# Kernel optimization log

Measured on AMD Instinct MI355X. Metric: run time of the kernel, lower is better.

Reference implementation:

```python
import jax, jax.numpy as jnp
import numpy as np

NUM_USERS = 100000
NUM_ITEMS = 50000
N_NODES = NUM_USERS + NUM_ITEMS
EMBED_K = 64
N_LAYERS = 3
N_EDGES = 2000000
BATCH = 4096
EPS = 1e-12
NEG_SLOPE = 0.01  # torch.nn.functional.leaky_relu default


def setup_inputs() -> dict:
    key = jax.random.key(0)
    ks = jax.random.split(key, 12)
    return {
        "Gu": jax.random.normal(ks[0], (NUM_USERS, EMBED_K), jnp.float32) * 0.1,
        "Gi": jax.random.normal(ks[1], (NUM_ITEMS, EMBED_K), jnp.float32) * 0.1,
        "W1": jax.random.normal(ks[2], (N_LAYERS, EMBED_K, EMBED_K), jnp.float32) * 0.1,
        "b1": jax.random.normal(ks[3], (N_LAYERS, EMBED_K), jnp.float32) * 0.1,
        "W2": jax.random.normal(ks[4], (N_LAYERS, EMBED_K, EMBED_K), jnp.float32) * 0.1,
        "b2": jax.random.normal(ks[5], (N_LAYERS, EMBED_K), jnp.float32) * 0.1,
        "edge_w": jax.random.uniform(ks[6], (N_EDGES,), jnp.float32),
        "edge_src": jax.random.randint(ks[7], (N_EDGES,), 0, N_NODES, jnp.int32),
        "edge_dst": jax.random.randint(ks[8], (N_EDGES,), 0, N_NODES, jnp.int32),
        "user": jax.random.randint(ks[9], (BATCH,), 0, NUM_USERS, jnp.int32),
        "pos": jax.random.randint(ks[10], (BATCH,), 0, NUM_ITEMS, jnp.int32),
    }


def _propagate(Gu, Gi, W1, b1, W2, b2, edge_w, edge_src, edge_dst):
    # ego embeddings: concat users then items -> [N, d]
    x = jnp.concatenate([Gu, Gi], axis=0)
    embs = [x]
    for l in range(N_LAYERS):
        xj = x[edge_src]                       # [E, d] source (neighbor) feats
        xi = x[edge_dst]                       # [E, d] destination feats
        # NGCF message: norm * (lin1(x_j) + lin2(x_j * x_i))
        msg = (xj @ W1[l] + b1[l]) + ((xj * xi) @ W2[l] + b2[l])
        msg = msg * edge_w[:, None]
        agg = jax.ops.segment_sum(msg, edge_dst, num_segments=N_NODES)
        # update: aggregated messages + self transform, then LeakyReLU
        out = jax.nn.leaky_relu(agg + x @ W1[l] + b1[l], negative_slope=NEG_SLOPE)
        # message dropout is identity in eval mode; then row-wise L2 normalize
        nrm = jnp.sqrt(jnp.sum(out * out, axis=1, keepdims=True))
        x = out / jnp.maximum(nrm, EPS)
        embs.append(x)
    all_e = jnp.concatenate(embs, axis=1)      # [N, d*(L+1)]
    return all_e[:NUM_USERS], all_e[NUM_USERS:]


def reference(Gu, Gi, W1, b1, W2, b2, edge_w, edge_src, edge_dst, user, pos):
    gu, gi = _propagate(Gu, Gi, W1, b1, W2, b2, edge_w, edge_src, edge_dst)
    gamma_u = gu[user]                         # [B, d*(L+1)]
    gamma_i = gi[pos]
    xui = jnp.sum(gamma_u * gamma_i, axis=1)   # [B]
    return xui
```

## Files before the change

### kernel.cpp

```cpp
#include <hip/hip_runtime.h>


#define SCAN_TILE 4096
#define LAYER_GRID 1536

__global__ __launch_bounds__(256) void init_x_kernel(
    const float* __restrict__ Gu, const float* __restrict__ Gi,
    float* __restrict__ x, int nu4, int nt4) {
  int i = blockIdx.x * 256 + threadIdx.x;
  if (i >= nt4) return;
  float4 v = (i < nu4) ? ((const float4*)Gu)[i] : ((const float4*)Gi)[i - nu4];
  ((float4*)x)[i] = v;
}

__global__ __launch_bounds__(256) void hist_kernel(
    const int* __restrict__ dst, int* __restrict__ counts, int E) {
  int e = blockIdx.x * 256 + threadIdx.x;
  if (e >= E) return;
  atomicAdd(&counts[dst[e]], 1);
}

__global__ __launch_bounds__(256) void tile_sum_kernel(
    const int* __restrict__ counts, int* __restrict__ tsum, int n) {
  int tid = threadIdx.x;
  int lo = blockIdx.x * SCAN_TILE + tid * 16;
  int s = 0;
  if (lo + 16 <= n) {
    const int4* p = (const int4*)(counts + lo);
#pragma unroll
    for (int q = 0; q < 4; ++q) {
      int4 v = p[q];
      s += v.x + v.y + v.z + v.w;
    }
  } else {
    for (int i = lo; i < n && i < lo + 16; ++i) s += counts[i];
  }
#pragma unroll
  for (int m = 1; m < 64; m <<= 1) s += __shfl_xor(s, m, 64);
  __shared__ int red[4];
  if ((tid & 63) == 0) red[tid >> 6] = s;
  __syncthreads();
  if (tid == 0) tsum[blockIdx.x] = red[0] + red[1] + red[2] + red[3];
}

__global__ __launch_bounds__(64) void tile_scan_kernel(int* __restrict__ tsum,
                                                       int ntiles) {
  int lane = threadIdx.x;
  if (ntiles <= 64) {
    int v = (lane < ntiles) ? tsum[lane] : 0;
    int incl = v;
#pragma unroll
    for (int m = 1; m < 64; m <<= 1) {
      int t = __shfl_up(incl, m, 64);
      if (lane >= m) incl += t;
    }
    if (lane < ntiles) tsum[lane] = incl - v;
  } else if (lane == 0) {
    int run = 0;
    for (int i = 0; i < ntiles; ++i) {
      int t = tsum[i];
      tsum[i] = run;
      run += t;
    }
  }
}

__global__ __launch_bounds__(256) void tile_write_kernel(
    const int* __restrict__ counts, const int* __restrict__ tsum,
    int* __restrict__ starts, int* __restrict__ cursor, int n) {
  int tid = threadIdx.x;
  int lo = blockIdx.x * SCAN_TILE + tid * 16;
  int c[16];
  int s = 0;
#pragma unroll
  for (int q = 0; q < 16; ++q) {
    int i = lo + q;
    int v = (i < n) ? counts[i] : 0;
    c[q] = v;
    s += v;
  }
  __shared__ int bs[256];
  bs[tid] = s;
  __syncthreads();
  int incl = s;
  for (int off = 1; off < 256; off <<= 1) {
    int t = (tid >= off) ? bs[tid - off] : 0;
    __syncthreads();
    incl += t;
    bs[tid] = incl;
    __syncthreads();
  }
  int run = tsum[blockIdx.x] + incl - s;
#pragma unroll
  for (int q = 0; q < 16; ++q) {
    int i = lo + q;
    if (i < n) {
      starts[i] = run;
      cursor[i] = run;
      run += c[q];
    }
  }
}

__global__ __launch_bounds__(256) void place_kernel(
    const int* __restrict__ src, const int* __restrict__ dst,
    const float* __restrict__ w, int* __restrict__ cursor,
    int2* __restrict__ ebuf, int E) {
  int e = blockIdx.x * 256 + threadIdx.x;
  if (e >= E) return;
  int p = atomicAdd(&cursor[dst[e]], 1);
  ebuf[p] = make_int2(src[e], __float_as_int(w[e]));
}

__global__ __launch_bounds__(256) void dot_kernel(
    const float* __restrict__ x, const int* __restrict__ user,
    const int* __restrict__ pos, float* __restrict__ out,
    int batch, int nusers, int accumulate) {
  int b = blockIdx.x * 4 + (threadIdx.x >> 6);
  int lane = threadIdx.x & 63;
  if (b >= batch) return;
  int u = user[b];
  int p = nusers + pos[b];
  float val = x[u * 64 + lane] * x[p * 64 + lane];
#pragma unroll
  for (int m = 1; m < 64; m <<= 1) val += __shfl_xor(val, m, 64);
  if (lane == 0) out[b] = accumulate ? (out[b] + val) : val;
}

__global__ __launch_bounds__(256) void layer_kernel(
    const float* __restrict__ xc, float* __restrict__ xn,
    const float* __restrict__ W1, const float* __restrict__ b1,
    const float* __restrict__ W2, const float* __restrict__ b2,
    const int* __restrict__ starts, const int* __restrict__ degs,
    const int2* __restrict__ ebuf, int nnodes) {
  const int lane = threadIdx.x & 63;
  const int wid = threadIdx.x >> 6;
  __shared__ float ash[4][64];
  __shared__ float gsh[4][64];

  float w1c[64], w2c[64];
#pragma unroll
  for (int j = 0; j < 64; ++j) {
    w1c[j] = W1[j * 64 + lane];
    w2c[j] = W2[j * 64 + lane];
  }
  const float b1k = b1[lane];
  const float b2k = b2[lane];

  const int wstride = LAYER_GRID * 4;
  for (int v = blockIdx.x * 4 + wid; v < nnodes; v += wstride) {
    const float xk = xc[v * 64 + lane];
    int s0 = __builtin_amdgcn_readfirstlane(starts[v]);
    int dg = __builtin_amdgcn_readfirstlane(degs[v]);
    int nl = dg < 64 ? dg : 64;

    int myidx = 0;
    float myw = 0.f;
    if (lane < nl) {
      int2 m = ebuf[s0 + lane];
      myidx = m.x << 6;
      myw = __int_as_float(m.y);
    }
    float wsum = myw;
#pragma unroll
    for (int m = 1; m < 64; m <<= 1) wsum += __shfl_xor(wsum, m, 64);

    float S = 0.f;
    int j = 0;
    for (; j + 8 <= nl; j += 8) {
      float vv[8], ww[8];
#pragma unroll
      for (int q = 0; q < 8; ++q) {
        int a = __builtin_amdgcn_readlane(myidx, j + q);
        ww[q] = __uint_as_float(
            __builtin_amdgcn_readlane(__float_as_uint(myw), j + q));
        vv[q] = xc[a + lane];
      }
#pragma unroll
      for (int q = 0; q < 8; ++q) S = fmaf(ww[q], vv[q], S);
    }
    for (; j < nl; ++j) {
      int a = __builtin_amdgcn_readlane(myidx, j);
      float w = __uint_as_float(
          __builtin_amdgcn_readlane(__float_as_uint(myw), j));
      S = fmaf(w, xc[a + lane], S);
    }
    for (int e = s0 + 64; e < s0 + dg; ++e) {
      int2 m = ebuf[e];
      float w = __int_as_float(m.y);
      wsum += w;
      S = fmaf(w, xc[(m.x << 6) + lane], S);
    }

    ash[wid][lane] = S + xk;
    gsh[wid][lane] = S * xk;
    asm volatile("" ::: "memory");

    float acc1 = 0.f, acc2 = 0.f;
#pragma unroll
    for (int q = 0; q < 16; ++q) {
      float4 av, gv;
      __builtin_memcpy(&av, &ash[wid][4 * q], 16);
      __builtin_memcpy(&gv, &gsh[wid][4 * q], 16);
      acc1 = fmaf(av.x, w1c[4 * q + 0], acc1);
      acc1 = fmaf(av.y, w1c[4 * q + 1], acc1);
      acc1 = fmaf(av.z, w1c[4 * q + 2], acc1);
      acc1 = fmaf(av.w, w1c[4 * q + 3], acc1);
      acc2 = fmaf(gv.x, w2c[4 * q + 0], acc2);
      acc2 = fmaf(gv.y, w2c[4 * q + 1], acc2);
      acc2 = fmaf(gv.z, w2c[4 * q + 2], acc2);
      acc2 = fmaf(gv.w, w2c[4 * q + 3], acc2);
    }
    const float cv = wsum;
    float pre = acc1 + acc2 + (cv + 1.0f) * b1k + cv * b2k;
    float o = (pre > 0.0f) ? pre : 0.01f * pre;
    float ss = o * o;
#pragma unroll
    for (int m = 1; m < 64; m <<= 1) ss += __shfl_xor(ss, m, 64);
    float nrm = sqrtf(ss);
    xn[v * 64 + lane] = o / fmaxf(nrm, 1e-12f);
  }
}

extern "C" void kernel_launch(void* const* d_in, const int* in_sizes, int n_in,
                              void* d_out, int out_size, void* d_ws, size_t ws_size,
                              hipStream_t stream) {
  const float* Gu = (const float*)d_in[0];
  const float* Gi = (const float*)d_in[1];
  const float* W1 = (const float*)d_in[2];
  const float* b1 = (const float*)d_in[3];
  const float* W2 = (const float*)d_in[4];
  const float* b2 = (const float*)d_in[5];
  const float* ew = (const float*)d_in[6];
  const int* esrc = (const int*)d_in[7];
  const int* edst = (const int*)d_in[8];
  const int* user = (const int*)d_in[9];
  const int* pos = (const int*)d_in[10];
  float* out = (float*)d_out;

  const int NU = in_sizes[0] / 64;
  const int NI = in_sizes[1] / 64;
  const int N = NU + NI;
  const int E = in_sizes[6];
  const int B = in_sizes[9];

  char* ws = (char*)d_ws;
  size_t off = 0;
  auto carve = [&](size_t bytes) -> void* {
    void* p = ws + off;
    off = (off + bytes + 255) & ~(size_t)255;
    return p;
  };
  float* x0 = (float*)carve((size_t)N * 64 * 4);
  float* x1 = (float*)carve((size_t)N * 64 * 4);
  int2* ebuf = (int2*)carve((size_t)E * 8);
  int* startsA = (int*)carve((size_t)N * 4);
  int* cursor = (int*)carve((size_t)N * 4);
  int* counts = (int*)carve((size_t)N * 4);
  const int ntiles = (N + SCAN_TILE - 1) / SCAN_TILE;
  int* tsum = (int*)carve((size_t)ntiles * 4);

  hipMemsetAsync(counts, 0, (size_t)N * 4, stream);

  hist_kernel<<<(E + 255) / 256, 256, 0, stream>>>(edst, counts, E);
  tile_sum_kernel<<<ntiles, 256, 0, stream>>>(counts, tsum, N);
  tile_scan_kernel<<<1, 64, 0, stream>>>(tsum, ntiles);
  tile_write_kernel<<<ntiles, 256, 0, stream>>>(counts, tsum, startsA, cursor, N);
  place_kernel<<<(E + 255) / 256, 256, 0, stream>>>(esrc, edst, ew, cursor, ebuf, E);

  int nt4 = N * 64 / 4;
  int nu4 = NU * 64 / 4;
  init_x_kernel<<<(nt4 + 255) / 256, 256, 0, stream>>>(Gu, Gi, x0, nu4, nt4);
  dot_kernel<<<(B + 3) / 4, 256, 0, stream>>>(x0, user, pos, out, B, NU, 0);

  float* xc = x0;
  float* xn = x1;
  for (int l = 0; l < 3; ++l) {
    layer_kernel<<<LAYER_GRID, 256, 0, stream>>>(xc, xn, W1 + l * 4096,
                                                 b1 + l * 64, W2 + l * 4096,
                                                 b2 + l * 64, startsA, counts,
                                                 ebuf, N);
    dot_kernel<<<(B + 3) / 4, 256, 0, stream>>>(xn, user, pos, out, B, NU, 1);
    float* t = xc;
    xc = xn;
    xn = t;
  }
}
```

Before: 931.6 us.

## Move layer weights to swizzled LDS and batch four nodes per wave

The W1/W2 columns that each lane kept in 128 registers now live in LDS as two XOR-swizzled 64x64 matrices, loaded once per block. Blocks grow to 512 threads, and each wave gathers four nodes before running the dense transform, so every weight read from LDS is reused across four nodes. The goal is to lower register pressure so more waves fit per CU and the memory-bound gather hides latency better. The cost is extra LDS traffic and about 40KB of shared memory per block, which may itself cap occupancy.

```diff
diff --git a/kernel.cpp b/kernel.cpp
--- a/kernel.cpp
+++ b/kernel.cpp
@@ -2,7 +2,7 @@
 
 
 #define SCAN_TILE 4096
-#define LAYER_GRID 1536
+#define LAYER_BLOCKS 768
 
 __global__ __launch_bounds__(256) void init_x_kernel(
     const float* __restrict__ Gu, const float* __restrict__ Gi,
@@ -127,98 +127,132 @@
   if (lane == 0) out[b] = accumulate ? (out[b] + val) : val;
 }
 
-__global__ __launch_bounds__(256) void layer_kernel(
+__global__ __launch_bounds__(512, 4) void layer_kernel(
     const float* __restrict__ xc, float* __restrict__ xn,
-    const float* __restrict__ W1, const float* __restrict__ b1,
-    const float* __restrict__ W2, const float* __restrict__ b2,
+    const float* __restrict__ W1g, const float* __restrict__ b1,
+    const float* __restrict__ W2g, const float* __restrict__ b2,
     const int* __restrict__ starts, const int* __restrict__ degs,
     const int2* __restrict__ ebuf, int nnodes) {
   const int lane = threadIdx.x & 63;
   const int wid = threadIdx.x >> 6;
-  __shared__ float ash[4][64];
-  __shared__ float gsh[4][64];
-
-  float w1c[64], w2c[64];
-#pragma unroll
-  for (int j = 0; j < 64; ++j) {
-    w1c[j] = W1[j * 64 + lane];
-    w2c[j] = W2[j * 64 + lane];
+  __shared__ float wlds[2][4096];
+  __shared__ float ash[8][4][64];
+  __shared__ float gsh[8][4][64];
+
+  {
+    const int k = threadIdx.x >> 3;
+    const int r = threadIdx.x & 7;
+#pragma unroll
+    for (int mtx = 0; mtx < 2; ++mtx) {
+      const float* Wg = mtx ? W2g : W1g;
+#pragma unroll
+      for (int qq = 0; qq < 2; ++qq) {
+        int q = r * 2 + qq;
+        float4 val;
+        val.x = Wg[(4 * q + 0) * 64 + k];
+        val.y = Wg[(4 * q + 1) * 64 + k];
+        val.z = Wg[(4 * q + 2) * 64 + k];
+        val.w = Wg[(4 * q + 3) * 64 + k];
+        *(float4*)&wlds[mtx][k * 64 + ((q ^ (k & 15)) << 2)] = val;
+      }
+    }
   }
   const float b1k = b1[lane];
   const float b2k = b2[lane];
-
-  const int wstride = LAYER_GRID * 4;
-  for (int v = blockIdx.x * 4 + wid; v < nnodes; v += wstride) {
-    const float xk = xc[v * 64 + lane];
-    int s0 = __builtin_amdgcn_readfirstlane(starts[v]);
-    int dg = __builtin_amdgcn_readfirstlane(degs[v]);
-    int nl = dg < 64 ? dg : 64;
-
-    int myidx = 0;
-    float myw = 0.f;
-    if (lane < nl) {
-      int2 m = ebuf[s0 + lane];
-      myidx = m.x << 6;
-      myw = __int_as_float(m.y);
-    }
-    float wsum = myw;
-#pragma unroll
-    for (int m = 1; m < 64; m <<= 1) wsum += __shfl_xor(wsum, m, 64);
-
-    float S = 0.f;
-    int j = 0;
-    for (; j + 8 <= nl; j += 8) {
-      float vv[8], ww[8];
-#pragma unroll
-      for (int q = 0; q < 8; ++q) {
-        int a = __builtin_amdgcn_readlane(myidx, j + q);
-        ww[q] = __uint_as_float(
-            __builtin_amdgcn_readlane(__float_as_uint(myw), j + q));
-        vv[q] = xc[a + lane];
-      }
-#pragma unroll
-      for (int q = 0; q < 8; ++q) S = fmaf(ww[q], vv[q], S);
-    }
-    for (; j < nl; ++j) {
-      int a = __builtin_amdgcn_readlane(myidx, j);
-      float w = __uint_as_float(
-          __builtin_amdgcn_readlane(__float_as_uint(myw), j));
-      S = fmaf(w, xc[a + lane], S);
-    }
-    for (int e = s0 + 64; e < s0 + dg; ++e) {
-      int2 m = ebuf[e];
-      float w = __int_as_float(m.y);
-      wsum += w;
-      S = fmaf(w, xc[(m.x << 6) + lane], S);
-    }
-
-    ash[wid][lane] = S + xk;
-    gsh[wid][lane] = S * xk;
+  __syncthreads();
+
+  const int wstride = LAYER_BLOCKS * 8 * 4;
+  for (int vbase = (blockIdx.x * 8 + wid) * 4; vbase < nnodes;
+       vbase += wstride) {
+    const int nv = min(4, nnodes - vbase);
+    float wsum[4];
+
+    for (int n = 0; n < nv; ++n) {
+      const int v = vbase + n;
+      const float xk = xc[v * 64 + lane];
+      int s0 = __builtin_amdgcn_readfirstlane(starts[v]);
+      int dg = __builtin_amdgcn_readfirstlane(degs[v]);
+      int nl = dg < 64 ? dg : 64;
+
+      int myidx = 0;
+      float myw = 0.f;
+      if (lane < nl) {
+        int2 m = ebuf[s0 + lane];
+        myidx = m.x << 6;
+        myw = __int_as_float(m.y);
+      }
+      float ws = myw;
+#pragma unroll
+      for (int m = 1; m < 64; m <<= 1) ws += __shfl_xor(ws, m, 64);
+
+      float S = 0.f;
+      int j = 0;
+      for (; j + 8 <= nl; j += 8) {
+        float vv[8], ww[8];
+#pragma unroll
+        for (int q = 0; q < 8; ++q) {
+          int a = __builtin_amdgcn_readlane(myidx, j + q);
+          ww[q] = __uint_as_float(
+              __builtin_amdgcn_readlane(__float_as_uint(myw), j + q));
+          vv[q] = xc[a + lane];
+        }
+#pragma unroll
+        for (int q = 0; q < 8; ++q) S = fmaf(ww[q], vv[q], S);
+      }
+      for (; j < nl; ++j) {
+        int a = __builtin_amdgcn_readlane(myidx, j);
+        float w = __uint_as_float(
+            __builtin_amdgcn_readlane(__float_as_uint(myw), j));
+        S = fmaf(w, xc[a + lane], S);
+      }
+      for (int e = s0 + 64; e < s0 + dg; ++e) {
+        int2 m = ebuf[e];
+        float w = __int_as_float(m.y);
+        ws += w;
+        S = fmaf(w, xc[(m.x << 6) + lane], S);
+      }
+      wsum[n] = ws;
+      ash[wid][n][lane] = S + xk;
+      gsh[wid][n][lane] = S * xk;
+    }
     asm volatile("" ::: "memory");
 
-    float acc1 = 0.f, acc2 = 0.f;
-#pragma unroll
+    float acc1[4] = {0.f, 0.f, 0.f, 0.f};
+    float acc2[4] = {0.f, 0.f, 0.f, 0.f};
+    const int swzbase = lane * 64;
+    const int ksw = lane & 15;
+#pragma unroll 4
     for (int q = 0; q < 16; ++q) {
-      float4 av, gv;
-      __builtin_memcpy(&av, &ash[wid][4 * q], 16);
-      __builtin_memcpy(&gv, &gsh[wid][4 * q], 16);
-      acc1 = fmaf(av.x, w1c[4 * q + 0], acc1);
-      acc1 = fmaf(av.y, w1c[4 * q + 1], acc1);
-      acc1 = fmaf(av.z, w1c[4 * q + 2], acc1);
-      acc1 = fmaf(av.w, w1c[4 * q + 3], acc1);
-      acc2 = fmaf(gv.x, w2c[4 * q + 0], acc2);
-      acc2 = fmaf(gv.y, w2c[4 * q + 1], acc2);
-      acc2 = fmaf(gv.z, w2c[4 * q + 2], acc2);
-      acc2 = fmaf(gv.w, w2c[4 * q + 3], acc2);
-    }
-    const float cv = wsum;
-    float pre = acc1 + acc2 + (cv + 1.0f) * b1k + cv * b2k;
-    float o = (pre > 0.0f) ? pre : 0.01f * pre;
-    float ss = o * o;
-#pragma unroll
-    for (int m = 1; m < 64; m <<= 1) ss += __shfl_xor(ss, m, 64);
-    float nrm = sqrtf(ss);
-    xn[v * 64 + lane] = o / fmaxf(nrm, 1e-12f);
+      float4 w1q, w2q, av, gv;
+      __builtin_memcpy(&w1q, &wlds[0][swzbase + ((q ^ ksw) << 2)], 16);
+      __builtin_memcpy(&w2q, &wlds[1][swzbase + ((q ^ ksw) << 2)], 16);
+#pragma unroll
+      for (int n = 0; n < 4; ++n) {
+        __builtin_memcpy(&av, &ash[wid][n][4 * q], 16);
+        __builtin_memcpy(&gv, &gsh[wid][n][4 * q], 16);
+        acc1[n] = fmaf(av.x, w1q.x, acc1[n]);
+        acc1[n] = fmaf(av.y, w1q.y, acc1[n]);
+        acc1[n] = fmaf(av.z, w1q.z, acc1[n]);
+        acc1[n] = fmaf(av.w, w1q.w, acc1[n]);
+        acc2[n] = fmaf(gv.x, w2q.x, acc2[n]);
+        acc2[n] = fmaf(gv.y, w2q.y, acc2[n]);
+        acc2[n] = fmaf(gv.z, w2q.z, acc2[n]);
+        acc2[n] = fmaf(gv.w, w2q.w, acc2[n]);
+      }
+    }
+
+#pragma unroll
+    for (int n = 0; n < 4; ++n) {
+      if (n >= nv) break;
+      const float cv = wsum[n];
+      float pre = acc1[n] + acc2[n] + (cv + 1.0f) * b1k + cv * b2k;
+      float o = (pre > 0.0f) ? pre : 0.01f * pre;
+      float ss = o * o;
+#pragma unroll
+      for (int m = 1; m < 64; m <<= 1) ss += __shfl_xor(ss, m, 64);
+      float nrm = sqrtf(ss);
+      xn[(vbase + n) * 64 + lane] = o / fmaxf(nrm, 1e-12f);
+    }
   }
 }
 
@@ -276,10 +310,10 @@
   float* xc = x0;
   float* xn = x1;
   for (int l = 0; l < 3; ++l) {
-    layer_kernel<<<LAYER_GRID, 256, 0, stream>>>(xc, xn, W1 + l * 4096,
-                                                 b1 + l * 64, W2 + l * 4096,
-                                                 b2 + l * 64, startsA, counts,
-                                                 ebuf, N);
+    layer_kernel<<<LAYER_BLOCKS, 512, 0, stream>>>(xc, xn, W1 + l * 4096,
+                                                   b1 + l * 64, W2 + l * 4096,
+                                                   b2 + l * 64, startsA, counts,
+                                                   ebuf, N);
     dot_kernel<<<(B + 3) / 4, 256, 0, stream>>>(xn, user, pos, out, B, NU, 1);
     float* t = xc;
     xc = xn;
```

Measured after the change: 960.6 us. +3.1%, slower.
